# Optimization experiments

Hardware: AMD Instinct MI355X
Metric: run time of the kernel (lower is better)

## Reference

```python
import jax, jax.numpy as jnp
import numpy as np

IN_DIM = 16384
OUT_DIM = 8192
BATCH = 1024
MASK_DENSITY = 0.05


def setup_inputs() -> dict:
    key = jax.random.key(0)
    k_x, k_w, k_b, k_m = jax.random.split(key, 4)
    x = jax.random.normal(k_x, (BATCH, IN_DIM), dtype=jnp.float32)
    # kaiming_uniform(a=sqrt(5)) == uniform(-1/sqrt(in), 1/sqrt(in))
    bound = 1.0 / np.sqrt(IN_DIM)
    weights = jax.random.uniform(k_w, (OUT_DIM, IN_DIM), dtype=jnp.float32,
                                 minval=-bound, maxval=bound)
    bias = jax.random.uniform(k_b, (OUT_DIM,), dtype=jnp.float32,
                              minval=-bound, maxval=bound)
    mask = (jax.random.uniform(k_m, (OUT_DIM, IN_DIM)) < MASK_DENSITY).astype(jnp.float32)
    return {"x": x, "weights": weights, "bias": bias, "mask": mask}


def reference(x, weights, bias, mask):
    # output = x @ (weights * mask)^T + bias   (F.linear semantics)
    masked_w = weights * mask  # [out, in]
    return jnp.einsum('bi,oi->bo', x, masked_w) + bias
```

## Files before the change

kernel.cpp:

```cpp
#include <hip/hip_runtime.h>


#define IN_DIM 16384
#define OUT_DIM 8192
#define BATCH 1024

#define BM 256
#define BN 256
#define BK 64
#define KSPLIT 2
#define K_HALF (IN_DIM / KSPLIT)
#define NT_K (K_HALF / BK)
#define NT256 (OUT_DIM / BN)
#define MT256 (BATCH / BM)

typedef __attribute__((ext_vector_type(8))) short bf16x8;
typedef __attribute__((ext_vector_type(4))) float f32x4;
typedef __attribute__((ext_vector_type(8))) unsigned short u16x8;

__device__ __forceinline__ unsigned short f2bf(float f) {
  unsigned int u = __float_as_uint(f);
  return (unsigned short)((u + 0x7fffu + ((u >> 16) & 1u)) >> 16);
}

#define GL16(g, l)                                                \
  __builtin_amdgcn_global_load_lds(                               \
      (const __attribute__((address_space(1))) void*)(g),         \
      (__attribute__((address_space(3))) void*)(l), 16, 0, 0)

__global__ __launch_bounds__(256) void prep_w_kernel(
    const f32x4* __restrict__ w, const f32x4* __restrict__ m,
    u16x8* __restrict__ out, int n8) {
  int i = blockIdx.x * blockDim.x + threadIdx.x;
  int stride = gridDim.x * blockDim.x;
  for (; i < n8; i += stride) {
    f32x4 w0 = __builtin_nontemporal_load(&w[2 * i]);
    f32x4 w1 = __builtin_nontemporal_load(&w[2 * i + 1]);
    f32x4 m0 = __builtin_nontemporal_load(&m[2 * i]);
    f32x4 m1 = __builtin_nontemporal_load(&m[2 * i + 1]);
    u16x8 o;
    o[0] = f2bf(w0[0] * m0[0]);
    o[1] = f2bf(w0[1] * m0[1]);
    o[2] = f2bf(w0[2] * m0[2]);
    o[3] = f2bf(w0[3] * m0[3]);
    o[4] = f2bf(w1[0] * m1[0]);
    o[5] = f2bf(w1[1] * m1[1]);
    o[6] = f2bf(w1[2] * m1[2]);
    o[7] = f2bf(w1[3] * m1[3]);
    __builtin_nontemporal_store(o, &out[i]);
  }
}

__global__ __launch_bounds__(256) void prep_x_kernel(
    const f32x4* __restrict__ x, u16x8* __restrict__ out, int n8) {
  int i = blockIdx.x * blockDim.x + threadIdx.x;
  int stride = gridDim.x * blockDim.x;
  for (; i < n8; i += stride) {
    f32x4 v0 = __builtin_nontemporal_load(&x[2 * i]);
    f32x4 v1 = __builtin_nontemporal_load(&x[2 * i + 1]);
    u16x8 o;
    o[0] = f2bf(v0[0]);
    o[1] = f2bf(v0[1]);
    o[2] = f2bf(v0[2]);
    o[3] = f2bf(v0[3]);
    o[4] = f2bf(v1[0]);
    o[5] = f2bf(v1[1]);
    o[6] = f2bf(v1[2]);
    o[7] = f2bf(v1[3]);
    __builtin_nontemporal_store(o, &out[i]);
  }
}

__global__ __launch_bounds__(256) void reduce_kernel(
    const f32x4* __restrict__ p0, const f32x4* __restrict__ p1,
    const f32x4* __restrict__ bias4, f32x4* __restrict__ out, int n4) {
  int i = blockIdx.x * blockDim.x + threadIdx.x;
  int stride = gridDim.x * blockDim.x;
  for (; i < n4; i += stride) {
    f32x4 a = p0[i];
    f32x4 b = p1[i];
    f32x4 c = bias4[i & (OUT_DIM / 4 - 1)];
    out[i] = a + b + c;
  }
}

__global__ __launch_bounds__(512, 2) void gemm256(
    const short* __restrict__ Ab, const short* __restrict__ Bb,
    float* __restrict__ out0, float* __restrict__ out1) {
  __shared__ short As[2][BM * BK];
  __shared__ short Bs[2][BN * BK];

  const int tid = threadIdx.x;
  const int lane = tid & 63;
  const int wv = tid >> 6;
  const int wr = wv >> 2;
  const int wc = wv & 3;
  const int fr = lane & 15;
  const int fq = lane >> 4;

  const int bid = blockIdx.x;
  const int nt = bid & (NT256 - 1);
  const int rest = bid >> 5;
  const int mt = rest >> 1;
  const int kh = rest & 1;
  const int row0 = mt * BM;
  const int col0 = nt * BN;
  const int kbase = kh * K_HALF;
  float* __restrict__ dst = kh ? out1 : out0;

  const int swz8 = ((tid & 7) ^ ((tid >> 3) & 7)) * 8;
  const short* srcA = Ab + (size_t)(row0 + (tid >> 3)) * IN_DIM + kbase + swz8;
  const short* srcB = Bb + (size_t)(col0 + (tid >> 3)) * IN_DIM + kbase + swz8;
  char* ldsA_w = (char*)As + wv * 1024;
  char* ldsB_w = (char*)Bs + wv * 1024;

  const int swzslot = (fq ^ (fr & 7)) * 16;
  const int Abase = (wr * 128 + fr) * 128 + swzslot;
  const int Bbase = (wc * 64 + fr) * 128 + swzslot;

  f32x4 acc[8][4];
#pragma unroll
  for (int i = 0; i < 8; ++i)
#pragma unroll
    for (int j = 0; j < 4; ++j) acc[i][j] = (f32x4)0.f;

#define STAGE(kt, c)                                                       \
  do {                                                                     \
    const size_t ko_ = (size_t)(kt)*BK;                                    \
    _Pragma("unroll") for (int i_ = 0; i_ < 4; ++i_)                       \
        GL16(srcA + (size_t)i_ * 64 * IN_DIM + ko_,                        \
             ldsA_w + (c)*32768 + i_ * 8192);                              \
    _Pragma("unroll") for (int i_ = 0; i_ < 4; ++i_)                       \
        GL16(srcB + (size_t)i_ * 64 * IN_DIM + ko_,                        \
             ldsB_w + (c)*32768 + i_ * 8192);                              \
  } while (0)

  STAGE(0, 0);
  for (int t = 0; t < NT_K; ++t) {
    const int cur = t & 1;
    if (t + 1 < NT_K) {
      STAGE(t + 1, cur ^ 1);
      asm volatile("s_waitcnt vmcnt(8)" ::: "memory");
    } else {
      asm volatile("s_waitcnt vmcnt(0)" ::: "memory");
    }
    __builtin_amdgcn_s_barrier();

    const char* tA = (const char*)As + cur * 32768;
    const char* tB = (const char*)Bs + cur * 32768;
#pragma unroll
    for (int ks = 0; ks < 2; ++ks) {
      const int off = ks << 6;
      bf16x8 aF[8], bF[4];
#pragma unroll
      for (int m = 0; m < 8; ++m)
        aF[m] = *(const bf16x8*)(tA + ((Abase ^ off) + m * 2048));
#pragma unroll
      for (int n = 0; n < 4; ++n)
        bF[n] = *(const bf16x8*)(tB + ((Bbase ^ off) + n * 2048));
      __builtin_amdgcn_s_setprio(1);
#pragma unroll
      for (int m = 0; m < 8; ++m)
#pragma unroll
        for (int n = 0; n < 4; ++n)
          acc[m][n] = __builtin_amdgcn_mfma_f32_16x16x32_bf16(aF[m], bF[n],
                                                              acc[m][n], 0, 0,
                                                              0);
      __builtin_amdgcn_s_setprio(0);
    }
    __builtin_amdgcn_s_barrier();
  }

#pragma unroll
  for (int m = 0; m < 8; ++m) {
#pragma unroll
    for (int n = 0; n < 4; ++n) {
      const int c = col0 + wc * 64 + n * 16 + fr;
      const int rb = row0 + wr * 128 + m * 16 + fq * 4;
#pragma unroll
      for (int tt = 0; tt < 4; ++tt)
        dst[(size_t)(rb + tt) * OUT_DIM + c] = acc[m][n][tt];
    }
  }
#undef STAGE
}

__global__ __launch_bounds__(256) void gemm128_fused(
    const float* __restrict__ X, const float* __restrict__ W,
    const float* __restrict__ Msk, const float* __restrict__ bias,
    float* __restrict__ out) {
  __shared__ short As[128 * BK];
  __shared__ short Bs[128 * BK];
  const int tid = threadIdx.x;
  const int lane = tid & 63;
  const int wv4 = tid >> 6;
  const int wm = wv4 >> 1;
  const int wn = wv4 & 1;
  const int fr = lane & 15;
  const int fq = lane >> 4;
  const int bid = blockIdx.x;
  const int nt = bid & 63;
  const int mt = bid >> 6;
  const int row0 = mt * 128;
  const int col0 = nt * 128;
  f32x4 acc[4][4];
#pragma unroll
  for (int i = 0; i < 4; ++i)
#pragma unroll
    for (int j = 0; j < 4; ++j) acc[i][j] = (f32x4)0.f;
  for (int kt = 0; kt < IN_DIM / BK; ++kt) {
    const int k0 = kt * BK;
    __syncthreads();
#pragma unroll
    for (int is = 0; is < 4; ++is) {
      const int e = (is * 256 + tid) * 8;
      const int r = e >> 6;
      const int kk = e & 63;
      {
        const float* src = X + (size_t)(row0 + r) * IN_DIM + k0 + kk;
        f32x4 a0 = *(const f32x4*)src;
        f32x4 a1 = *(const f32x4*)(src + 4);
        bf16x8 v;
        v[0] = (short)f2bf(a0[0]); v[1] = (short)f2bf(a0[1]);
        v[2] = (short)f2bf(a0[2]); v[3] = (short)f2bf(a0[3]);
        v[4] = (short)f2bf(a1[0]); v[5] = (short)f2bf(a1[1]);
        v[6] = (short)f2bf(a1[2]); v[7] = (short)f2bf(a1[3]);
        *(bf16x8*)&As[r * BK + kk] = v;
      }
      {
        const float* sw = W + (size_t)(col0 + r) * IN_DIM + k0 + kk;
        const float* sm = Msk + (size_t)(col0 + r) * IN_DIM + k0 + kk;
        f32x4 w0 = *(const f32x4*)sw;
        f32x4 w1 = *(const f32x4*)(sw + 4);
        f32x4 m0 = *(const f32x4*)sm;
        f32x4 m1 = *(const f32x4*)(sm + 4);
        bf16x8 v;
        v[0] = (short)f2bf(w0[0] * m0[0]); v[1] = (short)f2bf(w0[1] * m0[1]);
        v[2] = (short)f2bf(w0[2] * m0[2]); v[3] = (short)f2bf(w0[3] * m0[3]);
        v[4] = (short)f2bf(w1[0] * m1[0]); v[5] = (short)f2bf(w1[1] * m1[1]);
        v[6] = (short)f2bf(w1[2] * m1[2]); v[7] = (short)f2bf(w1[3] * m1[3]);
        *(bf16x8*)&Bs[r * BK + kk] = v;
      }
    }
    __syncthreads();
#pragma unroll
    for (int ks = 0; ks < 2; ++ks) {
      bf16x8 af[4], bf[4];
#pragma unroll
      for (int i = 0; i < 4; ++i)
        af[i] = *(const bf16x8*)&As[(wm * 64 + i * 16 + fr) * BK + ks * 32 + fq * 8];
#pragma unroll
      for (int j = 0; j < 4; ++j)
        bf[j] = *(const bf16x8*)&Bs[(wn * 64 + j * 16 + fr) * BK + ks * 32 + fq * 8];
#pragma unroll
      for (int i = 0; i < 4; ++i)
#pragma unroll
        for (int j = 0; j < 4; ++j)
          acc[i][j] = __builtin_amdgcn_mfma_f32_16x16x32_bf16(af[i], bf[j],
                                                              acc[i][j], 0, 0, 0);
    }
  }
#pragma unroll
  for (int j = 0; j < 4; ++j) {
    const int c = col0 + wn * 64 + j * 16 + fr;
    const float bv = bias[c];
#pragma unroll
    for (int i = 0; i < 4; ++i) {
      const int rb = row0 + wm * 64 + i * 16 + fq * 4;
#pragma unroll
      for (int tt = 0; tt < 4; ++tt)
        out[(size_t)(rb + tt) * OUT_DIM + c] = acc[i][j][tt] + bv;
    }
  }
}

extern "C" void kernel_launch(void* const* d_in, const int* in_sizes, int n_in,
                              void* d_out, int out_size, void* d_ws, size_t ws_size,
                              hipStream_t stream) {
  const float* x = (const float*)d_in[0];
  const float* w = (const float*)d_in[1];
  const float* bias = (const float*)d_in[2];
  const float* mask = (const float*)d_in[3];
  float* out = (float*)d_out;

  const size_t wm_elems = (size_t)OUT_DIM * IN_DIM;
  const size_t xb_elems = (size_t)BATCH * IN_DIM;
  const size_t out_elems = (size_t)BATCH * OUT_DIM;
  const size_t need_bf16 = (wm_elems + xb_elems) * sizeof(short);
  const size_t need_split = need_bf16 + out_elems * sizeof(float);

  if (ws_size >= need_split) {
    short* wmb = (short*)d_ws;
    short* xbb = wmb + wm_elems;
    float* p1 = (float*)((char*)d_ws + need_bf16);
    hipLaunchKernelGGL(prep_w_kernel, dim3(4096), dim3(256), 0, stream,
                       (const f32x4*)w, (const f32x4*)mask, (u16x8*)wmb,
                       (int)(wm_elems / 8));
    hipLaunchKernelGGL(prep_x_kernel, dim3(512), dim3(256), 0, stream,
                       (const f32x4*)x, (u16x8*)xbb, (int)(xb_elems / 8));
    hipLaunchKernelGGL(gemm256, dim3(KSPLIT * MT256 * NT256), dim3(512), 0,
                       stream, xbb, wmb, out, p1);
    hipLaunchKernelGGL(reduce_kernel, dim3(2048), dim3(256), 0, stream,
                       (const f32x4*)out, (const f32x4*)p1,
                       (const f32x4*)bias, (f32x4*)out, (int)(out_elems / 4));
  } else {
    hipLaunchKernelGGL(gemm128_fused, dim3(512), dim3(256), 0, stream, x, w,
                       mask, bias, out);
  }
}
```

Baseline: 596.0 us.

## Restructure gemm256 into 4-phase interleaved pipeline with B prefetched two tiles ahead

```diff
diff --git a/kernel.cpp b/kernel.cpp
--- a/kernel.cpp
+++ b/kernel.cpp
@@ -87,8 +87,8 @@
 __global__ __launch_bounds__(512, 2) void gemm256(
     const short* __restrict__ Ab, const short* __restrict__ Bb,
     float* __restrict__ out0, float* __restrict__ out1) {
-  __shared__ short As[2][BM * BK];
-  __shared__ short Bs[2][BN * BK];
+  __shared__ short As[2][2][128 * 64];
+  __shared__ short Bs[2][2][128 * 64];
 
   const int tid = threadIdx.x;
   const int lane = tid & 63;
@@ -97,6 +97,7 @@
   const int wc = wv & 3;
   const int fr = lane & 15;
   const int fq = lane >> 4;
+  const int wv8 = wv * 8;
 
   const int bid = blockIdx.x;
   const int nt = bid & (NT256 - 1);
@@ -111,12 +112,28 @@
   const int swz8 = ((tid & 7) ^ ((tid >> 3) & 7)) * 8;
   const short* srcA = Ab + (size_t)(row0 + (tid >> 3)) * IN_DIM + kbase + swz8;
   const short* srcB = Bb + (size_t)(col0 + (tid >> 3)) * IN_DIM + kbase + swz8;
-  char* ldsA_w = (char*)As + wv * 1024;
-  char* ldsB_w = (char*)Bs + wv * 1024;
+  char* ldsA = (char*)As;
+  char* ldsB = (char*)Bs;
+  const int stg = wv8 * 128;
+
+#define STAGE_A(h, kt, s)                                                  \
+  do {                                                                     \
+    GL16(srcA + (size_t)((h)*128) * IN_DIM + (size_t)(kt)*BK,              \
+         ldsA + (s)*32768 + (h)*16384 + stg);                              \
+    GL16(srcA + (size_t)((h)*128 + 64) * IN_DIM + (size_t)(kt)*BK,         \
+         ldsA + (s)*32768 + (h)*16384 + 8192 + stg);                       \
+  } while (0)
+#define STAGE_B(h, kt, s)                                                  \
+  do {                                                                     \
+    GL16(srcB + (size_t)((h)*128) * IN_DIM + (size_t)(kt)*BK,              \
+         ldsB + (s)*32768 + (h)*16384 + stg);                              \
+    GL16(srcB + (size_t)((h)*128 + 64) * IN_DIM + (size_t)(kt)*BK,         \
+         ldsB + (s)*32768 + (h)*16384 + 8192 + stg);                       \
+  } while (0)
 
   const int swzslot = (fq ^ (fr & 7)) * 16;
-  const int Abase = (wr * 128 + fr) * 128 + swzslot;
-  const int Bbase = (wc * 64 + fr) * 128 + swzslot;
+  const int Abase = wr * 16384 + fr * 128 + swzslot;
+  const int Bbase = (wc >> 1) * 16384 + (wc & 1) * 8192 + fr * 128 + swzslot;
 
   f32x4 acc[8][4];
 #pragma unroll
@@ -124,51 +141,68 @@
 #pragma unroll
     for (int j = 0; j < 4; ++j) acc[i][j] = (f32x4)0.f;
 
-#define STAGE(kt, c)                                                       \
-  do {                                                                     \
-    const size_t ko_ = (size_t)(kt)*BK;                                    \
-    _Pragma("unroll") for (int i_ = 0; i_ < 4; ++i_)                       \
-        GL16(srcA + (size_t)i_ * 64 * IN_DIM + ko_,                        \
-             ldsA_w + (c)*32768 + i_ * 8192);                              \
-    _Pragma("unroll") for (int i_ = 0; i_ < 4; ++i_)                       \
-        GL16(srcB + (size_t)i_ * 64 * IN_DIM + ko_,                        \
-             ldsB_w + (c)*32768 + i_ * 8192);                              \
-  } while (0)
-
-  STAGE(0, 0);
+  STAGE_A(0, 0, 0);
+  STAGE_A(1, 0, 0);
+  STAGE_B(0, 0, 0);
+  STAGE_B(1, 0, 0);
+  STAGE_B(0, 1, 1);
+  STAGE_B(1, 1, 1);
+  asm volatile("s_waitcnt vmcnt(4)" ::: "memory");
+  __builtin_amdgcn_s_barrier();
+
   for (int t = 0; t < NT_K; ++t) {
-    const int cur = t & 1;
-    if (t + 1 < NT_K) {
-      STAGE(t + 1, cur ^ 1);
-      asm volatile("s_waitcnt vmcnt(8)" ::: "memory");
-    } else {
-      asm volatile("s_waitcnt vmcnt(0)" ::: "memory");
-    }
-    __builtin_amdgcn_s_barrier();
-
-    const char* tA = (const char*)As + cur * 32768;
-    const char* tB = (const char*)Bs + cur * 32768;
-#pragma unroll
-    for (int ks = 0; ks < 2; ++ks) {
-      const int off = ks << 6;
-      bf16x8 aF[8], bF[4];
-#pragma unroll
-      for (int m = 0; m < 8; ++m)
-        aF[m] = *(const bf16x8*)(tA + ((Abase ^ off) + m * 2048));
-#pragma unroll
-      for (int n = 0; n < 4; ++n)
-        bF[n] = *(const bf16x8*)(tB + ((Bbase ^ off) + n * 2048));
+    const int s = t & 1;
+    const int o = s ^ 1;
+    const char* tA = (const char*)As + s * 32768;
+    const char* tB = (const char*)Bs + s * 32768;
+    bf16x8 bF[4][2];
+#pragma unroll
+    for (int q = 0; q < 4; ++q) {
+      bf16x8 aF[2][2];
+      if (q == 0) {
+#pragma unroll
+        for (int n = 0; n < 4; ++n)
+#pragma unroll
+          for (int ks = 0; ks < 2; ++ks)
+            bF[n][ks] =
+                *(const bf16x8*)(tB + ((Bbase + n * 2048) ^ (ks << 6)));
+      }
+#pragma unroll
+      for (int mi = 0; mi < 2; ++mi)
+#pragma unroll
+        for (int ks = 0; ks < 2; ++ks)
+          aF[mi][ks] = *(const bf16x8*)(tA + ((Abase + (q * 2 + mi) * 2048) ^
+                                              (ks << 6)));
+      if (q == 0) {
+        if (t + 1 < NT_K) {
+          STAGE_A(0, t + 1, o);
+          STAGE_A(1, t + 1, o);
+        }
+      } else if (q == 1) {
+        if (t + 2 < NT_K) STAGE_B(0, t + 2, s);
+      } else if (q == 2) {
+        if (t + 2 < NT_K) STAGE_B(1, t + 2, s);
+      } else {
+        if (t < NT_K - 2)
+          asm volatile("s_waitcnt vmcnt(4)" ::: "memory");
+        else
+          asm volatile("s_waitcnt vmcnt(0)" ::: "memory");
+      }
+      __builtin_amdgcn_s_barrier();
+      asm volatile("s_waitcnt lgkmcnt(0)" ::: "memory");
+      __builtin_amdgcn_sched_barrier(0);
       __builtin_amdgcn_s_setprio(1);
 #pragma unroll
-      for (int m = 0; m < 8; ++m)
-#pragma unroll
-        for (int n = 0; n < 4; ++n)
-          acc[m][n] = __builtin_amdgcn_mfma_f32_16x16x32_bf16(aF[m], bF[n],
-                                                              acc[m][n], 0, 0,
-                                                              0);
+      for (int ks = 0; ks < 2; ++ks)
+#pragma unroll
+        for (int mi = 0; mi < 2; ++mi)
+#pragma unroll
+          for (int n = 0; n < 4; ++n)
+            acc[q * 2 + mi][n] = __builtin_amdgcn_mfma_f32_16x16x32_bf16(
+                aF[mi][ks], bF[n][ks], acc[q * 2 + mi][n], 0, 0, 0);
       __builtin_amdgcn_s_setprio(0);
-    }
-    __builtin_amdgcn_s_barrier();
+      __builtin_amdgcn_s_barrier();
+    }
   }
 
 #pragma unroll
@@ -182,7 +216,8 @@
         dst[(size_t)(rb + tt) * OUT_DIM + c] = acc[m][n][tt];
     }
   }
-#undef STAGE
+#undef STAGE_A
+#undef STAGE_B
 }
 
 __global__ __launch_bounds__(256) void gemm128_fused(
```

Measured after the change: 600.6 us. No clear change (+0.8%).

## Restructure gemm256 main loop to stagger A/B staging and prefetch B fragments

Applied to the files above, without the earlier changes.

```diff
diff --git a/kernel.cpp b/kernel.cpp
--- a/kernel.cpp
+++ b/kernel.cpp
@@ -87,8 +87,8 @@
 __global__ __launch_bounds__(512, 2) void gemm256(
     const short* __restrict__ Ab, const short* __restrict__ Bb,
     float* __restrict__ out0, float* __restrict__ out1) {
-  __shared__ short As[2][BM * BK];
-  __shared__ short Bs[2][BN * BK];
+  __shared__ short As[2][256 * 64];
+  __shared__ short Bs[2][256 * 64];
 
   const int tid = threadIdx.x;
   const int lane = tid & 63;
@@ -111,8 +111,22 @@
   const int swz8 = ((tid & 7) ^ ((tid >> 3) & 7)) * 8;
   const short* srcA = Ab + (size_t)(row0 + (tid >> 3)) * IN_DIM + kbase + swz8;
   const short* srcB = Bb + (size_t)(col0 + (tid >> 3)) * IN_DIM + kbase + swz8;
-  char* ldsA_w = (char*)As + wv * 1024;
-  char* ldsB_w = (char*)Bs + wv * 1024;
+  char* ldsA = (char*)As;
+  char* ldsB = (char*)Bs;
+  const int stg = wv * 1024;
+
+#define STAGE_A(kt, s)                                                     \
+  do {                                                                     \
+    _Pragma("unroll") for (int i_ = 0; i_ < 4; ++i_)                       \
+        GL16(srcA + (size_t)(i_ * 64) * IN_DIM + (size_t)(kt)*BK,          \
+             ldsA + (s)*32768 + i_ * 8192 + stg);                          \
+  } while (0)
+#define STAGE_B(kt, s)                                                     \
+  do {                                                                     \
+    _Pragma("unroll") for (int i_ = 0; i_ < 4; ++i_)                       \
+        GL16(srcB + (size_t)(i_ * 64) * IN_DIM + (size_t)(kt)*BK,          \
+             ldsB + (s)*32768 + i_ * 8192 + stg);                          \
+  } while (0)
 
   const int swzslot = (fq ^ (fr & 7)) * 16;
   const int Abase = (wr * 128 + fr) * 128 + swzslot;
@@ -124,52 +138,57 @@
 #pragma unroll
     for (int j = 0; j < 4; ++j) acc[i][j] = (f32x4)0.f;
 
-#define STAGE(kt, c)                                                       \
+  bf16x8 bFv[4][2];
+
+#define TILE_BODY(T, S, O, DO_SA, DO_SB, VMN, DO_BF)                       \
   do {                                                                     \
-    const size_t ko_ = (size_t)(kt)*BK;                                    \
-    _Pragma("unroll") for (int i_ = 0; i_ < 4; ++i_)                       \
-        GL16(srcA + (size_t)i_ * 64 * IN_DIM + ko_,                        \
-             ldsA_w + (c)*32768 + i_ * 8192);                              \
-    _Pragma("unroll") for (int i_ = 0; i_ < 4; ++i_)                       \
-        GL16(srcB + (size_t)i_ * 64 * IN_DIM + ko_,                        \
-             ldsB_w + (c)*32768 + i_ * 8192);                              \
+    if (DO_SA) STAGE_A((T) + 1, O);                                        \
+    if (DO_SB) STAGE_B((T) + 2, S);                                        \
+    const char* tA_ = (const char*)As + (S)*32768;                         \
+    _Pragma("unroll") for (int m_ = 0; m_ < 8; ++m_) {                     \
+      bf16x8 a0_ = *(const bf16x8*)(tA_ + (Abase + m_ * 2048));            \
+      bf16x8 a1_ = *(const bf16x8*)(tA_ + ((Abase + m_ * 2048) ^ 64));     \
+      _Pragma("unroll") for (int n_ = 0; n_ < 4; ++n_) {                   \
+        acc[m_][n_] = __builtin_amdgcn_mfma_f32_16x16x32_bf16(             \
+            a0_, bFv[n_][0], acc[m_][n_], 0, 0, 0);                        \
+        acc[m_][n_] = __builtin_amdgcn_mfma_f32_16x16x32_bf16(             \
+            a1_, bFv[n_][1], acc[m_][n_], 0, 0, 0);                        \
+      }                                                                    \
+    }                                                                      \
+    asm volatile("s_waitcnt vmcnt(" #VMN ")" ::: "memory");                \
+    if (DO_BF) {                                                           \
+      const char* nB_ = (const char*)Bs + (O)*32768;                       \
+      _Pragma("unroll") for (int n_ = 0; n_ < 4; ++n_) {                   \
+        bFv[n_][0] = *(const bf16x8*)(nB_ + (Bbase + n_ * 2048));          \
+        bFv[n_][1] = *(const bf16x8*)(nB_ + ((Bbase + n_ * 2048) ^ 64));   \
+      }                                                                    \
+      asm volatile("s_waitcnt lgkmcnt(0)" ::: "memory");                   \
+    }                                                                      \
+    __builtin_amdgcn_s_barrier();                                          \
   } while (0)
 
-  STAGE(0, 0);
-  for (int t = 0; t < NT_K; ++t) {
-    const int cur = t & 1;
-    if (t + 1 < NT_K) {
-      STAGE(t + 1, cur ^ 1);
-      asm volatile("s_waitcnt vmcnt(8)" ::: "memory");
-    } else {
-      asm volatile("s_waitcnt vmcnt(0)" ::: "memory");
-    }
-    __builtin_amdgcn_s_barrier();
-
-    const char* tA = (const char*)As + cur * 32768;
-    const char* tB = (const char*)Bs + cur * 32768;
-#pragma unroll
-    for (int ks = 0; ks < 2; ++ks) {
-      const int off = ks << 6;
-      bf16x8 aF[8], bF[4];
-#pragma unroll
-      for (int m = 0; m < 8; ++m)
-        aF[m] = *(const bf16x8*)(tA + ((Abase ^ off) + m * 2048));
-#pragma unroll
-      for (int n = 0; n < 4; ++n)
-        bF[n] = *(const bf16x8*)(tB + ((Bbase ^ off) + n * 2048));
-      __builtin_amdgcn_s_setprio(1);
-#pragma unroll
-      for (int m = 0; m < 8; ++m)
-#pragma unroll
-        for (int n = 0; n < 4; ++n)
-          acc[m][n] = __builtin_amdgcn_mfma_f32_16x16x32_bf16(aF[m], bF[n],
-                                                              acc[m][n], 0, 0,
-                                                              0);
-      __builtin_amdgcn_s_setprio(0);
-    }
-    __builtin_amdgcn_s_barrier();
-  }
+  STAGE_A(0, 0);
+  STAGE_B(0, 0);
+  STAGE_B(1, 1);
+  asm volatile("s_waitcnt vmcnt(4)" ::: "memory");
+  __builtin_amdgcn_s_barrier();
+  {
+    const char* nB_ = (const char*)Bs;
+#pragma unroll
+    for (int n_ = 0; n_ < 4; ++n_) {
+      bFv[n_][0] = *(const bf16x8*)(nB_ + (Bbase + n_ * 2048));
+      bFv[n_][1] = *(const bf16x8*)(nB_ + ((Bbase + n_ * 2048) ^ 64));
+    }
+  }
+  asm volatile("s_waitcnt lgkmcnt(0)" ::: "memory");
+  __builtin_amdgcn_s_barrier();
+
+  for (int tt = 0; tt < NT_K - 2; tt += 2) {
+    TILE_BODY(tt, 0, 1, true, true, 4, true);
+    TILE_BODY(tt + 1, 1, 0, true, true, 4, true);
+  }
+  TILE_BODY(NT_K - 2, 0, 1, true, false, 0, true);
+  TILE_BODY(NT_K - 1, 1, 0, false, false, 0, false);
 
 #pragma unroll
   for (int m = 0; m < 8; ++m) {
@@ -182,7 +201,9 @@
         dst[(size_t)(rb + tt) * OUT_DIM + c] = acc[m][n][tt];
     }
   }
-#undef STAGE
+#undef TILE_BODY
+#undef STAGE_A
+#undef STAGE_B
 }
 
 __global__ __launch_bounds__(256) void gemm128_fused(
```

Result: faster. 581.0 us (-2.5%).

## Double gemm256 block to 16 waves with 64x64 per-wave tiles

Applied to the files above, without the earlier changes.

```diff
diff --git a/kernel.cpp b/kernel.cpp
--- a/kernel.cpp
+++ b/kernel.cpp
@@ -84,11 +84,11 @@
   }
 }
 
-__global__ __launch_bounds__(512, 2) void gemm256(
+__global__ __launch_bounds__(1024, 4) void gemm256(
     const short* __restrict__ Ab, const short* __restrict__ Bb,
     float* __restrict__ out0, float* __restrict__ out1) {
-  __shared__ short As[2][BM * BK];
-  __shared__ short Bs[2][BN * BK];
+  __shared__ short As[2][256 * 64];
+  __shared__ short Bs[2][256 * 64];
 
   const int tid = threadIdx.x;
   const int lane = tid & 63;
@@ -111,36 +111,43 @@
   const int swz8 = ((tid & 7) ^ ((tid >> 3) & 7)) * 8;
   const short* srcA = Ab + (size_t)(row0 + (tid >> 3)) * IN_DIM + kbase + swz8;
   const short* srcB = Bb + (size_t)(col0 + (tid >> 3)) * IN_DIM + kbase + swz8;
-  char* ldsA_w = (char*)As + wv * 1024;
-  char* ldsB_w = (char*)Bs + wv * 1024;
+  char* ldsA = (char*)As;
+  char* ldsB = (char*)Bs;
+  const int stg = wv * 1024;
+
+#define STAGE_A(KT, SL)                                                    \
+  do {                                                                     \
+    GL16(srcA + (size_t)(KT)*64, ldsA + (SL)*32768 + stg);                 \
+    GL16(srcA + (size_t)128 * IN_DIM + (size_t)(KT)*64,                    \
+         ldsA + (SL)*32768 + 16384 + stg);                                 \
+  } while (0)
+#define STAGE_B(KT, SL)                                                    \
+  do {                                                                     \
+    GL16(srcB + (size_t)(KT)*64, ldsB + (SL)*32768 + stg);                 \
+    GL16(srcB + (size_t)128 * IN_DIM + (size_t)(KT)*64,                    \
+         ldsB + (SL)*32768 + 16384 + stg);                                 \
+  } while (0)
 
   const int swzslot = (fq ^ (fr & 7)) * 16;
-  const int Abase = (wr * 128 + fr) * 128 + swzslot;
+  const int Abase = (wr * 64 + fr) * 128 + swzslot;
   const int Bbase = (wc * 64 + fr) * 128 + swzslot;
 
-  f32x4 acc[8][4];
-#pragma unroll
-  for (int i = 0; i < 8; ++i)
+  f32x4 acc[4][4];
+#pragma unroll
+  for (int i = 0; i < 4; ++i)
 #pragma unroll
     for (int j = 0; j < 4; ++j) acc[i][j] = (f32x4)0.f;
 
-#define STAGE(kt, c)                                                       \
-  do {                                                                     \
-    const size_t ko_ = (size_t)(kt)*BK;                                    \
-    _Pragma("unroll") for (int i_ = 0; i_ < 4; ++i_)                       \
-        GL16(srcA + (size_t)i_ * 64 * IN_DIM + ko_,                        \
-             ldsA_w + (c)*32768 + i_ * 8192);                              \
-    _Pragma("unroll") for (int i_ = 0; i_ < 4; ++i_)                       \
-        GL16(srcB + (size_t)i_ * 64 * IN_DIM + ko_,                        \
-             ldsB_w + (c)*32768 + i_ * 8192);                              \
-  } while (0)
-
-  STAGE(0, 0);
+  STAGE_A(0, 0);
+  STAGE_B(0, 0);
+
+#pragma unroll 1
   for (int t = 0; t < NT_K; ++t) {
     const int cur = t & 1;
     if (t + 1 < NT_K) {
-      STAGE(t + 1, cur ^ 1);
-      asm volatile("s_waitcnt vmcnt(8)" ::: "memory");
+      STAGE_A(t + 1, cur ^ 1);
+      STAGE_B(t + 1, cur ^ 1);
+      asm volatile("s_waitcnt vmcnt(4)" ::: "memory");
     } else {
       asm volatile("s_waitcnt vmcnt(0)" ::: "memory");
     }
@@ -151,46 +158,44 @@
 #pragma unroll
     for (int ks = 0; ks < 2; ++ks) {
       const int off = ks << 6;
-      bf16x8 aF[8], bF[4];
-#pragma unroll
-      for (int m = 0; m < 8; ++m)
-        aF[m] = *(const bf16x8*)(tA + ((Abase ^ off) + m * 2048));
+      bf16x8 bF[4];
 #pragma unroll
       for (int n = 0; n < 4; ++n)
-        bF[n] = *(const bf16x8*)(tB + ((Bbase ^ off) + n * 2048));
-      __builtin_amdgcn_s_setprio(1);
-#pragma unroll
-      for (int m = 0; m < 8; ++m)
+        bF[n] = *(const bf16x8*)(tB + ((Bbase + n * 2048) ^ off));
+#pragma unroll
+      for (int m = 0; m < 4; ++m) {
+        bf16x8 aF = *(const bf16x8*)(tA + ((Abase + m * 2048) ^ off));
 #pragma unroll
         for (int n = 0; n < 4; ++n)
-          acc[m][n] = __builtin_amdgcn_mfma_f32_16x16x32_bf16(aF[m], bF[n],
+          acc[m][n] = __builtin_amdgcn_mfma_f32_16x16x32_bf16(aF, bF[n],
                                                               acc[m][n], 0, 0,
                                                               0);
-      __builtin_amdgcn_s_setprio(0);
+      }
     }
     __builtin_amdgcn_s_barrier();
   }
 
 #pragma unroll
-  for (int m = 0; m < 8; ++m) {
+  for (int m = 0; m < 4; ++m) {
 #pragma unroll
     for (int n = 0; n < 4; ++n) {
       const int c = col0 + wc * 64 + n * 16 + fr;
-      const int rb = row0 + wr * 128 + m * 16 + fq * 4;
+      const int rb = row0 + wr * 64 + m * 16 + fq * 4;
 #pragma unroll
       for (int tt = 0; tt < 4; ++tt)
         dst[(size_t)(rb + tt) * OUT_DIM + c] = acc[m][n][tt];
     }
   }
-#undef STAGE
+#undef STAGE_A
+#undef STAGE_B
 }
 
 __global__ __launch_bounds__(256) void gemm128_fused(
     const float* __restrict__ X, const float* __restrict__ W,
     const float* __restrict__ Msk, const float* __restrict__ bias,
     float* __restrict__ out) {
-  __shared__ short As[128 * BK];
-  __shared__ short Bs[128 * BK];
+  __shared__ short As[128 * 64];
+  __shared__ short Bs[128 * 64];
   const int tid = threadIdx.x;
   const int lane = tid & 63;
   const int wv4 = tid >> 6;
@@ -208,8 +213,8 @@
   for (int i = 0; i < 4; ++i)
 #pragma unroll
     for (int j = 0; j < 4; ++j) acc[i][j] = (f32x4)0.f;
-  for (int kt = 0; kt < IN_DIM / BK; ++kt) {
-    const int k0 = kt * BK;
+  for (int kt = 0; kt < IN_DIM / 64; ++kt) {
+    const int k0 = kt * 64;
     __syncthreads();
 #pragma unroll
     for (int is = 0; is < 4; ++is) {
@@ -225,7 +230,7 @@
         v[2] = (short)f2bf(a0[2]); v[3] = (short)f2bf(a0[3]);
         v[4] = (short)f2bf(a1[0]); v[5] = (short)f2bf(a1[1]);
         v[6] = (short)f2bf(a1[2]); v[7] = (short)f2bf(a1[3]);
-        *(bf16x8*)&As[r * BK + kk] = v;
+        *(bf16x8*)&As[r * 64 + kk] = v;
       }
       {
         const float* sw = W + (size_t)(col0 + r) * IN_DIM + k0 + kk;
@@ -239,7 +244,7 @@
         v[2] = (short)f2bf(w0[2] * m0[2]); v[3] = (short)f2bf(w0[3] * m0[3]);
         v[4] = (short)f2bf(w1[0] * m1[0]); v[5] = (short)f2bf(w1[1] * m1[1]);
         v[6] = (short)f2bf(w1[2] * m1[2]); v[7] = (short)f2bf(w1[3] * m1[3]);
-        *(bf16x8*)&Bs[r * BK + kk] = v;
+        *(bf16x8*)&Bs[r * 64 + kk] = v;
       }
     }
     __syncthreads();
@@ -248,10 +253,10 @@
       bf16x8 af[4], bf[4];
 #pragma unroll
       for (int i = 0; i < 4; ++i)
-        af[i] = *(const bf16x8*)&As[(wm * 64 + i * 16 + fr) * BK + ks * 32 + fq * 8];
+        af[i] = *(const bf16x8*)&As[(wm * 64 + i * 16 + fr) * 64 + ks * 32 + fq * 8];
 #pragma unroll
       for (int j = 0; j < 4; ++j)
-        bf[j] = *(const bf16x8*)&Bs[(wn * 64 + j * 16 + fr) * BK + ks * 32 + fq * 8];
+        bf[j] = *(const bf16x8*)&Bs[(wn * 64 + j * 16 + fr) * 64 + ks * 32 + fq * 8];
 #pragma unroll
       for (int i = 0; i < 4; ++i)
 #pragma unroll
@@ -298,7 +303,7 @@
                        (int)(wm_elems / 8));
     hipLaunchKernelGGL(prep_x_kernel, dim3(512), dim3(256), 0, stream,
                        (const f32x4*)x, (u16x8*)xbb, (int)(xb_elems / 8));
-    hipLaunchKernelGGL(gemm256, dim3(KSPLIT * MT256 * NT256), dim3(512), 0,
+    hipLaunchKernelGGL(gemm256, dim3(KSPLIT * MT256 * NT256), dim3(1024), 0,
                        stream, xbb, wmb, out, p1);
     hipLaunchKernelGGL(reduce_kernel, dim3(2048), dim3(256), 0, stream,
                        (const f32x4*)out, (const f32x4*)p1,
```

Result: faster. 551.6 us, median of 2 (-7.4%).
